# Kernel tuning notes

Measured on AMD Instinct MI355X. Metric: run time of the kernel, lower is better.

## Reference

```python
import jax, jax.numpy as jnp
import numpy as np
from jax import lax

# ---- fake-quant helpers (brevitas-style per-tensor float scaling, STE round) ----
EPS = 1e-8

def _ste_round(x):
    return x + lax.stop_gradient(jnp.round(x) - x)

def _scale(x, qmax):
    s = lax.stop_gradient(jnp.max(jnp.abs(x))) / qmax
    return jnp.maximum(s, EPS)

def fq(x, scale, qmin, qmax):
    # fake-quantize: round-to-nearest with straight-through estimator, clip, dequant
    return jnp.clip(_ste_round(x / scale), qmin, qmax) * scale

def quant_act_int8(x):
    s = _scale(x, 127.0)
    return fq(x, s, -128.0, 127.0), s

def quant_weight_int4(w):
    # 4-bit signed, narrow range [-7, 7] (brevitas weight quant default narrow_range)
    s = _scale(w, 7.0)
    return fq(w, s, -7.0, 7.0), s

def quant_relu_uint4(x):
    y = jax.nn.relu(x)
    s = _scale(y, 15.0)
    return fq(y, s, 0.0, 15.0)

def quant_bias_int32(b, scale):
    # Int32Bias: bias quantized at input_scale * weight_scale
    return _ste_round(b / scale) * scale

def conv2d_same(x, w):
    # NCHW, OIHW, padding=1, stride=1
    return lax.conv_general_dilated(x, w, window_strides=(1, 1), padding=((1, 1), (1, 1)),
                                    dimension_numbers=('NCHW', 'OIHW', 'NCHW'))

def maxpool2(x):
    return lax.reduce_window(x, -jnp.inf, lax.max, (1, 1, 2, 2), (1, 1, 2, 2), 'VALID')

def quant_conv(x, w, b):
    xq, sx = quant_act_int8(x)        # input_quant: Int8ActPerTensorFloat
    wq, sw = quant_weight_int4(w)     # weight_bit_width=4
    bq = quant_bias_int32(b, sx * sw) # bias_quant: Int32Bias
    y = conv2d_same(xq, wq) + bq[None, :, None, None]
    yq, _ = quant_act_int8(y)         # output_quant: Int8ActPerTensorFloat
    return yq

def quant_linear(x, w, b):
    xq, sx = quant_act_int8(x)
    wq, sw = quant_weight_int4(w)
    bq = quant_bias_int32(b, sx * sw)
    y = xq @ wq.T + bq
    yq, _ = quant_act_int8(y)
    return yq


def setup_inputs() -> dict:
    key = jax.random.key(0)
    ks = jax.random.split(key, 7)
    B = 8192
    x = jax.random.normal(ks[0], (B, 1, 28, 28), dtype=jnp.float32)
    w1 = jax.random.normal(ks[1], (16, 1, 3, 3), dtype=jnp.float32) * 0.3
    b1 = jax.random.normal(ks[2], (16,), dtype=jnp.float32) * 0.1
    w2 = jax.random.normal(ks[3], (32, 16, 3, 3), dtype=jnp.float32) * 0.1
    b2 = jax.random.normal(ks[4], (32,), dtype=jnp.float32) * 0.1
    wf = jax.random.normal(ks[5], (10, 32 * 7 * 7), dtype=jnp.float32) * 0.05
    bf = jax.random.normal(ks[6], (10,), dtype=jnp.float32) * 0.1
    return {'x': x, 'w1': w1, 'b1': b1, 'w2': w2, 'b2': b2, 'wf': wf, 'bf': bf}


def reference(x, w1, b1, w2, b2, wf, bf):
    h, _ = quant_act_int8(x)              # inputQuant
    h = quant_conv(h, w1, b1)             # conv1
    h = quant_relu_uint4(h)               # relu1 (4-bit)
    h = maxpool2(h)                       # pool1 -> [B,16,14,14]
    h = quant_conv(h, w2, b2)             # conv2
    h = quant_relu_uint4(h)               # relu2
    h = maxpool2(h)                       # pool2 -> [B,32,7,7]
    h = h.reshape(h.shape[0], -1)         # flatten -> [B,1568]
    return quant_linear(h, wf, bf)        # fc -> [B,10]
```

## Files before the change

kernel.cpp:

```cpp
#include <hip/hip_runtime.h>
#include <climits>

#define NB 8192
#define EPSQ 1e-8f

using i32x4  = __attribute__((ext_vector_type(4)))  int;
using i32x16 = __attribute__((ext_vector_type(16))) int;

#define WS_F(ws)     ((float*)(ws))
#define WS_I(ws)     ((int*)((char*)(ws)+128))
#define WS_B1L(ws)   ((int*)((char*)(ws)+384))
#define WS_B2L(ws)   ((int*)((char*)(ws)+448))
#define WS_BFL(ws)   ((int*)((char*)(ws)+576))
#define WS_M1F(ws)   ((float*)((char*)(ws)+640))
#define WS_B1F(ws)   ((float*)((char*)(ws)+1280))
#define WS_B2FR(ws)  ((char*)(ws)+2048)
#define WS_Q2TAB(ws) ((signed char*)((char*)(ws)+7168))
#define WS_Q3TAB(ws) ((signed char*)((char*)(ws)+7424))
#define WS_B1FR(ws)  ((char*)(ws)+7680)
#define WS_MFF(ws)   ((float*)((char*)(ws)+20480))
#define WS_WFP(ws)   ((char*)(ws)+83200)
#define WS_RA1(ws)   ((int*)((char*)(ws)+139264))
#define WS_RS1(ws)   ((int*)((char*)(ws)+164352))
#define WS_RA2(ws)   ((int*)((char*)(ws)+189440))
#define WS_RS2(ws)   ((int*)((char*)(ws)+197632))
#define WS_RA3(ws)   ((int*)((char*)(ws)+205824))
#define WS_RAX(ws)   ((float*)((char*)(ws)+206848))
#define WS_WMX(ws)   ((float*)((char*)(ws)+215040))
#define WS_Q2B(ws)   ((signed char*)((char*)(ws)+215552))
#define WS_BIG_OFF   281600

__device__ __forceinline__ float clampf(float v, float lo, float hi){ return fminf(fmaxf(v, lo), hi); }

__device__ __forceinline__ float wave_max_f(float v){
#pragma unroll
  for (int off=32; off; off>>=1) v = fmaxf(v, __shfl_down(v, off, 64));
  return v;
}
__device__ __forceinline__ int wave_max_i(int v){
#pragma unroll
  for (int off=32; off; off>>=1) v = max(v, __shfl_down(v, off, 64));
  return v;
}

__device__ __forceinline__ void reduce2_atomic(int amax, int smax, int* gA, int* gS){
  amax = wave_max_i(amax); smax = wave_max_i(smax);
  __shared__ int sA[4], sS[4];
  int w = threadIdx.x>>6, l = threadIdx.x&63;
  if (l==0){ sA[w]=amax; sS[w]=smax; }
  __syncthreads();
  if (threadIdx.x==0){
#pragma unroll
    for (int i=1;i<4;i++){ amax=max(amax,sA[i]); smax=max(smax,sS[i]); }
    atomicMax(gA, amax); atomicMax(gS, smax);
  }
}

__device__ __forceinline__ void reduce2_store(int amax, int smax, int* pA, int* pS){
  amax = wave_max_i(amax); smax = wave_max_i(smax);
  __shared__ int sA[4], sS[4];
  int w = threadIdx.x>>6, l = threadIdx.x&63;
  if (l==0){ sA[w]=amax; sS[w]=smax; }
  __syncthreads();
  if (threadIdx.x==0){
#pragma unroll
    for (int i=1;i<4;i++){ amax=max(amax,sA[i]); smax=max(smax,sS[i]); }
    *pA = amax; *pS = smax;
  }
}

__global__ void k_init(char* ws){
  int* I = WS_I(ws);
  if (threadIdx.x==0){ I[0]=0; I[1]=0; I[2]=INT_MIN; I[3]=0; I[4]=INT_MIN; I[5]=0; }
}

__global__ void k_absx(const float* __restrict__ x, char* ws){
  const float4* x4 = (const float4*)x;
  const int n4 = NB*784/4;
  float m = 0.f;
  for (int i = blockIdx.x*blockDim.x + threadIdx.x; i < n4; i += gridDim.x*blockDim.x){
    float4 v = x4[i];
    m = fmaxf(m, fmaxf(fmaxf(fabsf(v.x),fabsf(v.y)), fmaxf(fabsf(v.z),fabsf(v.w))));
  }
  m = wave_max_f(m);
  __shared__ float sm[4];
  int w = threadIdx.x>>6;
  if ((threadIdx.x&63)==0) sm[w]=m;
  __syncthreads();
  if (threadIdx.x==0){
    m = fmaxf(fmaxf(sm[0],sm[1]), fmaxf(sm[2],sm[3]));
    WS_RAX(ws)[blockIdx.x] = m;
  }
}

__global__ void k_absxw(const float* __restrict__ x,
                        const float* __restrict__ w1, const float* __restrict__ w2,
                        const float* __restrict__ wf, char* ws){
  __shared__ float red[256];
  int b = blockIdx.x, t = threadIdx.x;
  if (b < 81){
    float m = 0.f;
    if (b==0){ if (t<144) m = fabsf(w1[t]); }
    else if (b<19){ m = fabsf(w2[(b-1)*256 + t]); }
    else { int i=(b-19)*256+t; if (i<15680) m = fabsf(wf[i]); }
    red[t]=m; __syncthreads();
    for (int s=128;s;s>>=1){ if (t<s) red[t]=fmaxf(red[t],red[t+s]); __syncthreads(); }
    if (t==0) WS_WMX(ws)[b]=red[0];
    return;
  }
  const int xb = b - 81;
  const float4* x4 = (const float4*)x;
  const int n4 = NB*784/4;
  float m = 0.f;
  for (int i = xb*256 + t; i < n4; i += 2048*256){
    float4 v = x4[i];
    m = fmaxf(m, fmaxf(fmaxf(fabsf(v.x),fabsf(v.y)), fmaxf(fabsf(v.z),fabsf(v.w))));
  }
  m = wave_max_f(m);
  __shared__ float sm[4];
  int w = t>>6;
  if ((t&63)==0) sm[w]=m;
  __syncthreads();
  if (t==0){
    m = fmaxf(fmaxf(sm[0],sm[1]), fmaxf(sm[2],sm[3]));
    WS_RAX(ws)[xb] = m;
  }
}

__global__ void k_wmax(const float* __restrict__ w1, const float* __restrict__ w2,
                       const float* __restrict__ wf, char* ws){
  __shared__ float red[256];
  int b = blockIdx.x, t = threadIdx.x;
  float m = 0.f;
  if (b==0){ if (t<144) m = fabsf(w1[t]); }
  else if (b<19){ m = fabsf(w2[(b-1)*256 + t]); }
  else { int i=(b-19)*256+t; if (i<15680) m = fabsf(wf[i]); }
  red[t]=m; __syncthreads();
  for (int s=128;s;s>>=1){ if (t<s) red[t]=fmaxf(red[t],red[t+s]); __syncthreads(); }
  if (t==0) WS_WMX(ws)[b]=red[0];
}

__global__ void k_scales(const float* __restrict__ w1, const float* __restrict__ b1, char* ws){
  __shared__ float red[256];
  float* F = WS_F(ws);
  int t = threadIdx.x;
  float vw1 = WS_WMX(ws)[0];
  float m2=0.f, mf=0.f;
  if (t<18) m2 = WS_WMX(ws)[1+t];
  if (t<62) mf = WS_WMX(ws)[19+t];
  red[t]=m2; __syncthreads();
  for (int s=128;s;s>>=1){ if (t<s) red[t]=fmaxf(red[t],red[t+s]); __syncthreads(); }
  float mw2=red[0]; __syncthreads();
  red[t]=mf; __syncthreads();
  for (int s=128;s;s>>=1){ if (t<s) red[t]=fmaxf(red[t],red[t+s]); __syncthreads(); }
  float mwf=red[0]; __syncthreads();
  float mxv=0.f;
  for (int i=t;i<2048;i+=256) mxv=fmaxf(mxv,WS_RAX(ws)[i]);
  red[t]=mxv; __syncthreads();
  for (int s=128;s;s>>=1){ if (t<s) red[t]=fmaxf(red[t],red[t+s]); __syncthreads(); }
  float mx=red[0]; __syncthreads();

  float s0  = fmaxf(mx/127.f, EPSQ);
  float sx1 = fmaxf((127.f*s0)/127.f, EPSQ);
  float sw1 = fmaxf(vw1/7.f, EPSQ);
  float sw2 = fmaxf(mw2/7.f, EPSQ);
  float swf = fmaxf(mwf/7.f, EPSQ);
  float sb1 = sx1*sw1;
  if (t==0){ F[0]=s0; F[1]=sx1; F[2]=sw1; F[3]=sb1; F[7]=sw2; F[12]=swf; }
  if (t<144) WS_M1F(ws)[t] = clampf(rintf(w1[t]/sw1), -7.f, 7.f);
  if (t<16){
    int bl = (int)rintf(b1[t]/sb1);
    WS_B1L(ws)[t] = bl;
    WS_B1F(ws)[t] = (float)bl;
  }
}

__global__ void k_pack(const float* __restrict__ w1, const float* __restrict__ w2,
                       const float* __restrict__ wf, char* ws){
  const float* F = WS_F(ws);
  int id = blockIdx.x*256 + threadIdx.x;
  if (id < 5120){
    float sw2 = F[7];
    int chunk=id>>10, r=id&1023, ln=r>>4, j=r&15;
    int tap=2*chunk+(ln>>5), oc=ln&31;
    signed char v=0;
    if (tap<9) v=(signed char)clampf(rintf(w2[oc*144 + j*9 + tap]/sw2), -7.f, 7.f);
    WS_B2FR(ws)[id]=v;
  } else if (id < 6144){
    float sw1 = F[2];
    int i=id-5120;
    int ln=i>>4, j=i&15;
    int k=(ln>>5)*16+j, oc=ln&31;
    signed char v=0;
    if (k<9 && oc<16) v=(signed char)clampf(rintf(w1[oc*9+k]/sw1), -7.f, 7.f);
    WS_B1FR(ws)[i]=v;
  } else if (id < 56320){
    float swf = F[12];
    int i=id-6144;
    int chunk=i>>10, r2=i&1023, ln=r2>>4, j=r2&15;
    int oc=ln&31, k=chunk*32+(ln>>5)*16+j;
    int cell=k>>5, ch=k&31;
    signed char v=0;
    if (oc<10) v=(signed char)clampf(rintf(wf[oc*1568 + ch*49 + cell]/swf), -7.f, 7.f);
    ((signed char*)WS_WFP(ws))[i]=v;
  } else if (id < 72000){
    float swf = F[12];
    int i=id-56320;
    WS_MFF(ws)[i] = clampf(rintf(wf[i]/swf), -7.f, 7.f);
  }
}

__global__ void k_wq(const float* __restrict__ w1, const float* __restrict__ b1,
                     const float* __restrict__ w2, const float* __restrict__ wf,
                     char* ws){
  __shared__ float red[256];
  float* F = WS_F(ws);
  int t = threadIdx.x;
  auto bmaxabs = [&](const float* p, int n)->float{
    float m=0.f; for (int i=t;i<n;i+=256) m=fmaxf(m,fabsf(p[i]));
    red[t]=m; __syncthreads();
    for (int s=128;s;s>>=1){ if (t<s) red[t]=fmaxf(red[t],red[t+s]); __syncthreads(); }
    float r=red[0]; __syncthreads(); return r;
  };
  float mw1 = bmaxabs(w1,144);
  float mw2 = bmaxabs(w2,4608);
  float mwf = bmaxabs(wf,15680);
  float mxv=0.f;
  for (int i=t;i<2048;i+=256) mxv=fmaxf(mxv,WS_RAX(ws)[i]);
  red[t]=mxv; __syncthreads();
  for (int s=128;s;s>>=1){ if (t<s) red[t]=fmaxf(red[t],red[t+s]); __syncthreads(); }
  float mx=red[0]; __syncthreads();

  float s0  = fmaxf(mx/127.f, EPSQ);
  float sx1 = fmaxf((127.f*s0)/127.f, EPSQ);
  float sw1 = fmaxf(mw1/7.f, EPSQ);
  float sw2 = fmaxf(mw2/7.f, EPSQ);
  float swf = fmaxf(mwf/7.f, EPSQ);
  float sb1 = sx1*sw1;
  if (t==0){ F[0]=s0; F[1]=sx1; F[2]=sw1; F[3]=sb1; F[7]=sw2; F[12]=swf; }
  float* m1f = WS_M1F(ws);
  for (int i=t;i<144;i+=256) m1f[i] = clampf(rintf(w1[i]/sw1), -7.f, 7.f);
  if (t<16){
    int bl = (int)rintf(b1[t]/sb1);
    WS_B1L(ws)[t] = bl;
    WS_B1F(ws)[t] = (float)bl;
  }
  for (int i=t;i<5120;i+=256){
    int chunk=i>>10, r=i&1023, ln=r>>4, j=r&15;
    int tap=2*chunk+(ln>>5), oc=ln&31;
    signed char v=0;
    if (tap<9) v=(signed char)clampf(rintf(w2[oc*144 + j*9 + tap]/sw2), -7.f, 7.f);
    WS_B2FR(ws)[i]=v;
  }
  for (int i=t;i<1024;i+=256){
    int ln=i>>4, j=i&15;
    int k=(ln>>5)*16+j, oc=ln&31;
    signed char v=0;
    if (k<9 && oc<16) v=(signed char)clampf(rintf(w1[oc*9+k]/sw1), -7.f, 7.f);
    WS_B1FR(ws)[i]=v;
  }
  float* mff = WS_MFF(ws);
  for (int i=t;i<15680;i+=256) mff[i] = clampf(rintf(wf[i]/swf), -7.f, 7.f);
  for (int i=t;i<50176;i+=256){
    int chunk=i>>10, r2=i&1023, ln=r2>>4, j=r2&15;
    int oc=ln&31, k=chunk*32+(ln>>5)*16+j;
    int cell=k>>5, ch=k&31;
    signed char v=0;
    if (oc<10) v=(signed char)clampf(rintf(wf[oc*1568 + ch*49 + cell]/swf), -7.f, 7.f);
    ((signed char*)WS_WFP(ws))[i]=v;
  }
}

template<bool FULLR>
__global__ void k_s1(const float* __restrict__ b2, char* ws){
  float* F=WS_F(ws); int* I=WS_I(ws);
  __shared__ int rA[256], rS[256];
  __shared__ float sh[4];
  int t=threadIdx.x;
  int amaxI, smaxI;
  if constexpr (FULLR){
    int a=0, s=INT_MIN;
    const int* ra=WS_RA1(ws); const int* rs=WS_RS1(ws);
    for (int i=t;i<6272;i+=256){ a=max(a,ra[i]); s=max(s,rs[i]); }
    rA[t]=a; rS[t]=s; __syncthreads();
    for (int st=128;st;st>>=1){ if (t<st){ rA[t]=max(rA[t],rA[t+st]); rS[t]=max(rS[t],rS[t+st]); } __syncthreads(); }
    amaxI=rA[0]; smaxI=rS[0];
  } else { amaxI=I[1]; smaxI=I[2]; }
  if (t==0){
    float sb1=F[3];
    float sy1 = fmaxf((sb1*(float)amaxI)/127.f, EPSQ);
    float mp  = sb1*(float)smaxI;
    float P1  = clampf(rintf(mp/sy1), 0.f, 127.f);
    float sr1 = fmaxf((sy1*P1)/15.f, EPSQ);
    float N1  = clampf(rintf((sy1*P1)/sr1), 0.f, 15.f);
    float sx2 = fmaxf((N1*sr1)/127.f, EPSQ);
    float sb2 = sx2*F[7];
    F[4]=sy1; F[5]=sr1; F[6]=sx2; F[8]=sb2;
    sh[0]=sy1; sh[1]=sr1; sh[2]=sx2; sh[3]=sb2;
  }
  __syncthreads();
  float sy1=sh[0], sr1=sh[1], sx2=sh[2], sb2=sh[3];
  int k = t-128;
  float n = (k>0) ? clampf(rintf((sy1*(float)k)/sr1), 0.f, 15.f) : 0.f;
  WS_Q2TAB(ws)[t] = (signed char)clampf(rintf((n*sr1)/sx2), -128.f, 127.f);
  if (t<32) WS_B2L(ws)[t] = (int)rintf(b2[t]/sb2);
}

__global__ void k_s1q2(const float* __restrict__ b2, char* ws){
  float* F=WS_F(ws);
  __shared__ int rA[256], rS[256];
  int t=threadIdx.x;
  int a=0, s=INT_MIN;
  const int* ra=WS_RA1(ws); const int* rs=WS_RS1(ws);
  for (int i=t;i<6272;i+=256){ a=max(a,ra[i]); s=max(s,rs[i]); }
  rA[t]=a; rS[t]=s; __syncthreads();
  for (int st=128;st;st>>=1){ if (t<st){ rA[t]=max(rA[t],rA[t+st]); rS[t]=max(rS[t],rS[t+st]); } __syncthreads(); }
  int amaxI=rA[0], smaxI=rS[0];
  float sb1=F[3];
  float sy1 = fmaxf((sb1*(float)amaxI)/127.f, EPSQ);
  float P1  = clampf(rintf((sb1*(float)smaxI)/sy1), 0.f, 127.f);
  float sr1 = fmaxf((sy1*P1)/15.f, EPSQ);
  float N1  = clampf(rintf((sy1*P1)/sr1), 0.f, 15.f);
  float sx2 = fmaxf((N1*sr1)/127.f, EPSQ);
  float sb2 = sx2*F[7];
  if (blockIdx.x==0){
    if (t==0){ F[4]=sy1; F[5]=sr1; F[6]=sx2; F[8]=sb2; }
    if (t<32) WS_B2L(ws)[t] = (int)rintf(b2[t]/sb2);
  }
  int idx = blockIdx.x*256 + t;
  int m = idx - 32768;
  float k1 = clampf(rintf((sb1*(float)m)/sy1), -128.f, 127.f);
  float n  = (k1>0.f) ? clampf(rintf((sy1*k1)/sr1), 0.f, 15.f) : 0.f;
  WS_Q2B(ws)[idx] = (signed char)clampf(rintf((n*sr1)/sx2), -128.f, 127.f);
}

template<bool FULLR>
__global__ void k_s2(const float* __restrict__ bf, char* ws){
  float* F=WS_F(ws); int* I=WS_I(ws);
  __shared__ int rA[256], rS[256];
  __shared__ float sh[4];
  int t=threadIdx.x;
  int amaxI, smaxI;
  if constexpr (FULLR){
    int a=0, s=INT_MIN;
    const int* ra=WS_RA2(ws); const int* rs=WS_RS2(ws);
    for (int i=t;i<2048;i+=256){ a=max(a,ra[i]); s=max(s,rs[i]); }
    rA[t]=a; rS[t]=s; __syncthreads();
    for (int st=128;st;st>>=1){ if (t<st){ rA[t]=max(rA[t],rA[t+st]); rS[t]=max(rS[t],rS[t+st]); } __syncthreads(); }
    amaxI=rA[0]; smaxI=rS[0];
  } else { amaxI=I[3]; smaxI=I[4]; }
  if (t==0){
    float sb2=F[8];
    float sy2 = fmaxf((sb2*(float)amaxI)/127.f, EPSQ);
    float mp  = sb2*(float)smaxI;
    float P2  = clampf(rintf(mp/sy2), 0.f, 127.f);
    float sr2 = fmaxf((sy2*P2)/15.f, EPSQ);
    float N2  = clampf(rintf((sy2*P2)/sr2), 0.f, 15.f);
    float sx3 = fmaxf((N2*sr2)/127.f, EPSQ);
    float sb3 = sx3*F[12];
    F[9]=sy2; F[10]=sr2; F[11]=sx3; F[13]=sb3;
    sh[0]=sy2; sh[1]=sr2; sh[2]=sx3; sh[3]=sb3;
  }
  __syncthreads();
  float sy2=sh[0], sr2=sh[1], sx3=sh[2], sb3=sh[3];
  int k = t-128;
  float n = (k>0) ? clampf(rintf((sy2*(float)k)/sr2), 0.f, 15.f) : 0.f;
  WS_Q3TAB(ws)[t] = (signed char)clampf(rintf((n*sr2)/sx3), -128.f, 127.f);
  if (t<16) WS_BFL(ws)[t] = (t<10) ? (int)rintf(bf[t]/sb3) : 0;
}

template<bool FULLR>
__global__ void k_s3(char* ws){
  float* F=WS_F(ws); int* I=WS_I(ws);
  __shared__ int rA[256];
  int t=threadIdx.x;
  int amaxI;
  if constexpr (FULLR){
    rA[t] = WS_RA3(ws)[t];
    __syncthreads();
    for (int st=128;st;st>>=1){ if (t<st) rA[t]=max(rA[t],rA[t+st]); __syncthreads(); }
    amaxI = rA[0];
  } else { amaxI = I[5]; }
  if (t==0) F[14] = fmaxf((F[13]*(float)amaxI)/127.f, EPSQ);
}

__global__ __launch_bounds__(256) void k_conv1f(const float* __restrict__ x,
                                                char* __restrict__ ws,
                                                short* __restrict__ i1p){
  const int t = threadIdx.x;
  const int id = blockIdx.x*256 + t;
  const int img = id/196, cell = id - img*196;
  const int py = cell/14, px = cell - py*14;
  const float s0 = WS_F(ws)[0];
  const float* xi = x + img*784;
  const int r0 = 2*py-1, c0 = 2*px-1;
  float in[4][4];
#pragma unroll
  for (int rr=0; rr<4; rr++){
    int r = r0+rr;
    bool rv = (unsigned)r < 28u;
#pragma unroll
    for (int cc=0; cc<4; cc++){
      int c = c0+cc;
      float v = 0.f;
      if (rv && (unsigned)c < 28u) v = xi[r*28+c];
      in[rr][cc] = v;
    }
  }
#pragma unroll
  for (int rr=0; rr<4; rr++)
#pragma unroll
    for (int cc=0; cc<4; cc++)
      in[rr][cc] = clampf(rintf(in[rr][cc]/s0), -128.f, 127.f);

  const float* __restrict__ m1f = WS_M1F(ws);
  const float* __restrict__ b1f = WS_B1F(ws);
  int amax=0, smax=INT_MIN;
  short outv[16];
#pragma unroll
  for (int oc=0; oc<16; oc++){
    float b = b1f[oc];
    float a00=b, a01=b, a10=b, a11=b;
#pragma unroll
    for (int dy=0; dy<3; dy++){
#pragma unroll
      for (int dx=0; dx<3; dx++){
        float wt = m1f[oc*9+dy*3+dx];
        a00 = fmaf(in[dy  ][dx  ], wt, a00);
        a01 = fmaf(in[dy  ][dx+1], wt, a01);
        a10 = fmaf(in[dy+1][dx  ], wt, a10);
        a11 = fmaf(in[dy+1][dx+1], wt, a11);
      }
    }
    int v00=(int)a00, v01=(int)a01, v10=(int)a10, v11=(int)a11;
    int mx = max(max(v00,v01), max(v10,v11));
    int ax = max(max(v00<0?-v00:v00, v01<0?-v01:v01), max(v10<0?-v10:v10, v11<0?-v11:v11));
    amax = max(amax, ax);
    smax = max(smax, mx);
    outv[oc] = (short)mx;
  }
  int4* dst = (int4*)(i1p + (size_t)id*16);
  dst[0] = *(const int4*)&outv[0];
  dst[1] = *(const int4*)&outv[8];
  reduce2_store(amax, smax, &WS_RA1(ws)[blockIdx.x], &WS_RS1(ws)[blockIdx.x]);
}

__global__ __launch_bounds__(256) void k_conv2r(char* __restrict__ ws,
                                                short* __restrict__ i1p,
                                                int* __restrict__ p2g){
  __shared__ __align__(16) signed char q2p4[4][4096];
  const int t=threadIdx.x, lane=t&63, wid=t>>6;
  const int img = blockIdx.x*4 + wid;
  signed char* q2p = q2p4[wid];
  const signed char* __restrict__ q2b = WS_Q2B(ws);

#pragma unroll
  for (int k=0;k<8;k++) ((unsigned long long*)q2p)[lane + 64*k] = 0ULL;

  const unsigned* src = (const unsigned*)(i1p + (size_t)img*3136);
#pragma unroll
  for (int k=0;k<24;k++){
    int idx = lane + 64*k;
    unsigned wv = src[idx];
    int e0 = idx*2;
    int cellc = e0 >> 4, ch = e0 & 15;
    int pyc = cellc/14, pxc = cellc - pyc*14;
    int m0 = (int)(short)(wv & 0xFFFFu);
    int m1 = (int)(short)(wv >> 16);
    int b0 = (int)(unsigned char)q2b[m0+32768];
    int b1 = (int)(unsigned char)q2b[m1+32768];
    *(unsigned short*)(q2p + ((pyc+1)*16 + (pxc+1))*16 + ch) = (unsigned short)(b0 | (b1<<8));
  }
  if (lane < 32){
    int idx = 1536 + lane;
    unsigned wv = src[idx];
    int e0 = idx*2;
    int cellc = e0 >> 4, ch = e0 & 15;
    int pyc = cellc/14, pxc = cellc - pyc*14;
    int m0 = (int)(short)(wv & 0xFFFFu);
    int m1 = (int)(short)(wv >> 16);
    int b0 = (int)(unsigned char)q2b[m0+32768];
    int b1 = (int)(unsigned char)q2b[m1+32768];
    *(unsigned short*)(q2p + ((pyc+1)*16 + (pxc+1))*16 + ch) = (unsigned short)(b0 | (b1<<8));
  }

  i32x4 bfr[5];
  const i32x4* bg = (const i32x4*)WS_B2FR(ws);
#pragma unroll
  for (int c=0;c<5;c++) bfr[c] = bg[c*64+lane];
  const int col = lane&31, h = lane>>5;
  const int bias = WS_B2L(ws)[col];
  int amax2=0, smax2=INT_MIN;
  const int TOFF[9] = {0,1,2,16,17,18,32,33,34};
  int* dstb = p2g + (size_t)img*1568;

#pragma unroll
  for (int mt=0; mt<7; mt++){
    int m = mt*32 + col;
    int g = m>>2, sub = m&3;
    bool gv = g < 49;
    int py = (g*37)>>8;
    int px = g - py*7;
    int oy = 2*py + (sub>>1), ox = 2*px + (sub&1);
    int E0 = oy*16 + ox;
    i32x16 acc;
#pragma unroll
    for (int r=0;r<16;r++) acc[r] = bias;
#pragma unroll
    for (int c=0;c<5;c++){
      const int t0 = TOFF[2*c];
      const int t1 = (2*c+1<9) ? TOFF[2*c+1] : -1;
      int toff = h ? t1 : t0;
      int entry = (gv && toff>=0) ? (E0 + toff) : 0;
      i32x4 a = *(const i32x4*)(q2p + entry*16);
      acc = __builtin_amdgcn_mfma_i32_32x32x32_i8(a, bfr[c], acc, 0,0,0);
    }
#pragma unroll
    for (int i=0;i<4;i++){
      int gg = mt*8 + 2*i + h;
      if (gg < 49){
        int v0=acc[4*i], v1=acc[4*i+1], v2=acc[4*i+2], v3=acc[4*i+3];
        int a0=v0<0?-v0:v0, a1=v1<0?-v1:v1, a2=v2<0?-v2:v2, a3=v3<0?-v3:v3;
        amax2 = max(amax2, max(max(a0,a1),max(a2,a3)));
        int mx = max(max(v0,v1),max(v2,v3));
        smax2 = max(smax2, mx);
        dstb[gg*32 + col] = mx;
      }
    }
  }
  reduce2_store(amax2, smax2, &WS_RA2(ws)[blockIdx.x], &WS_RS2(ws)[blockIdx.x]);
}

__global__ void k_rq2(const char* __restrict__ ws, const int* __restrict__ p2g,
                      signed char* __restrict__ q3g){
  const float* F = (const float*)ws;
  const float sb2 = F[8], sy2 = F[9];
  const signed char* q3t = WS_Q3TAB(ws);
  int id = blockIdx.x*256 + threadIdx.x;
  i32x4 m4 = ((const i32x4*)p2g)[id];
  unsigned out=0;
#pragma unroll
  for (int j=0;j<4;j++){
    float k2 = clampf(rintf((sb2*(float)m4[j])/sy2), -128.f, 127.f);
    out |= ((unsigned)(unsigned char)q3t[(int)k2+128]) << (8*j);
  }
  ((unsigned*)q3g)[id] = out;
}

__global__ __launch_bounds__(256) void k_fc(char* __restrict__ ws,
                                            const signed char* __restrict__ q3g,
                                            int* __restrict__ i3out){
  __shared__ int part[3][16][64];
  int t=threadIdx.x, lane=t&63, wid=t>>6;
  int mt = blockIdx.x;
  const int col=lane&31, h=lane>>5;
  const signed char* A0 = q3g + (size_t)(mt*32 + col)*1568 + 16*h;
  const i32x4* wfp = (const i32x4*)WS_WFP(ws);
  i32x16 acc;
#pragma unroll
  for (int r=0;r<16;r++) acc[r]=0;
#pragma unroll
  for (int cc=0; cc<13; cc++){
    int c = wid + cc*4;
    if (c < 49){
      i32x4 a = *(const i32x4*)(A0 + c*32);
      i32x4 b = wfp[c*64 + lane];
      acc = __builtin_amdgcn_mfma_i32_32x32x32_i8(a, b, acc, 0,0,0);
    }
  }
  if (wid>0){
#pragma unroll
    for (int r=0;r<16;r++) part[wid-1][r][lane] = acc[r];
  }
  __syncthreads();
  if (wid==0){
    int bias = (col<10) ? WS_BFL(ws)[col] : 0;
    int am=0;
#pragma unroll
    for (int r=0;r<16;r++){
      int v = acc[r] + part[0][r][lane] + part[1][r][lane] + part[2][r][lane] + bias;
      int row=(r&3)+8*(r>>2)+4*h;
      int img = mt*32+row;
      if (col<10){
        i3out[img*10+col] = v;
        am = max(am, v<0?-v:v);
      }
    }
    am = wave_max_i(am);
    if (lane==0) WS_RA3(ws)[blockIdx.x] = am;
  }
}

__global__ void k_out2(char* __restrict__ ws, float* __restrict__ out){
  __shared__ int rA[256];
  int t=threadIdx.x;
  rA[t] = WS_RA3(ws)[t];
  __syncthreads();
  for (int st=128;st;st>>=1){ if (t<st) rA[t]=max(rA[t],rA[t+st]); __syncthreads(); }
  float sb3 = WS_F(ws)[13];
  float sy3 = fmaxf((sb3*(float)rA[0])/127.f, EPSQ);
  int i = blockIdx.x*256 + t;
  if (i < NB*10){
    int iv = ((const int*)out)[i];
    float y = sb3*(float)iv;
    float q = clampf(rintf(y/sy3), -128.f, 127.f);
    out[i] = q*sy3;
  }
}

__global__ __launch_bounds__(256) void k_c1(const float* __restrict__ x, char* __restrict__ ws,
                                            short* __restrict__ i1p){
  constexpr int OFF_K0=0, OFF_A=960, OFF_I1=13760, OFF_B1=38848;
  __shared__ __align__(16) char arena[38912];
  signed char* k0b = (signed char*)(arena+OFF_K0);
  signed char* Abuf= (signed char*)(arena+OFF_A);
  short*       I1s = (short*)(arena+OFF_I1);
  int*         b1i = (int*)(arena+OFF_B1);

  const int tid=threadIdx.x, img=blockIdx.x;
  const int lane=tid&63, wid=tid>>6;
  const float s0 = WS_F(ws)[0];

  if (tid<16) b1i[tid]=WS_B1L(ws)[tid];
  for (int i=tid;i<240;i+=256) ((int*)k0b)[i]=0;
  for (int i=tid;i<3200;i+=256) ((int*)Abuf)[i]=0;
  __syncthreads();
  const float* xi = x + img*784;
  for (int i=tid;i<784;i+=256){
    int r=i/28, c=i-r*28;
    float v = clampf(rintf(xi[i]/s0), -128.f, 127.f);
    k0b[(r+1)*32 + (c+1)] = (signed char)v;
  }
  __syncthreads();
  for (int p=tid;p<784;p+=256){
    int oy=p/28, ox=p-oy*28;
    int base = oy*32+ox;
    int al = base & ~3, sh = (base&3)*8;
    unsigned l0a=*(const unsigned*)(k0b+al),    l1a=*(const unsigned*)(k0b+al+4);
    unsigned l0b=*(const unsigned*)(k0b+al+32), l1b=*(const unsigned*)(k0b+al+36);
    unsigned l0c=*(const unsigned*)(k0b+al+64), l1c=*(const unsigned*)(k0b+al+68);
    unsigned u0=(unsigned)(((((unsigned long long)l1a)<<32)|l0a)>>sh);
    unsigned u1=(unsigned)(((((unsigned long long)l1b)<<32)|l0b)>>sh);
    unsigned u2=(unsigned)(((((unsigned long long)l1c)<<32)|l0c)>>sh);
    i32x4 row;
    row[0]=(int)((u0&0xFFFFFFu)|(u1<<24));
    row[1]=(int)(((u1>>8)&0xFFFFu)|((u2&0xFFFFu)<<16));
    row[2]=(int)((u2>>16)&0xFFu);
    row[3]=0;
    *(i32x4*)(Abuf + p*16) = row;
  }
  __syncthreads();
  const i32x4 bfr = ((const i32x4*)WS_B1FR(ws))[lane];
  const int col=lane&31, h=lane>>5;
  const int bias=(col<16)? b1i[col] : 0;
  int amax=0, smax=INT_MIN;
  for (int mt=wid; mt<25; mt+=4){
    i32x4 a={0,0,0,0};
    if (h==0) a = *(const i32x4*)(Abuf + (mt*32+col)*16);
    i32x16 acc;
#pragma unroll
    for (int r=0;r<16;r++) acc[r]=bias;
    acc=__builtin_amdgcn_mfma_i32_32x32x32_i8(a,bfr,acc,0,0,0);
#pragma unroll
    for (int r=0;r<16;r++){
      int row=(r&3)+8*(r>>2)+4*h;
      int p=mt*32+row;
      if (p<784 && col<16){
        int v=acc[r];
        amax=max(amax,v<0?-v:v); smax=max(smax,v);
        I1s[p*16+col]=(short)v;
      }
    }
  }
  __syncthreads();
  for (int i=tid;i<3136;i+=256){
    int pp=i>>4, c=i&15, py=pp/14, px=pp-py*14;
    int p0=py*56+px*2;
    int m=max(max((int)I1s[p0*16+c],(int)I1s[(p0+1)*16+c]),
              max((int)I1s[(p0+28)*16+c],(int)I1s[(p0+29)*16+c]));
    i1p[(size_t)img*3136 + i]=(short)m;
  }
  reduce2_atomic(amax,smax,&WS_I(ws)[1],&WS_I(ws)[2]);
}

template<bool FIN>
__global__ __launch_bounds__(256) void k_c2(char* __restrict__ ws, const short* __restrict__ i1p,
                                            int* __restrict__ i3out){
  constexpr int OFF_Q2L=0, OFF_B2I=3136, OFF_Q2T=3264, OFF_N2=3520,
                OFF_Q3T=9792, OFF_BFS=10048, OFF_Q3F=10112, OFF_RED=16384;
  constexpr int ARENA = FIN ? 16544 : 3520;
  __shared__ __align__(16) char arena[ARENA];
  signed char* q2l=(signed char*)(arena+OFF_Q2L);
  int* b2li=(int*)(arena+OFF_B2I);
  signed char* q2t=(signed char*)(arena+OFF_Q2T);

  const int tid=threadIdx.x, img=blockIdx.x;
  const int lane=tid&63, wid=tid>>6;
  const float* F=WS_F(ws);
  const float sb1=F[3], sy1=F[4];

  q2t[tid]=WS_Q2TAB(ws)[tid];
  if (tid<32) b2li[tid]=WS_B2L(ws)[tid];
  if constexpr (FIN){
    ((signed char*)(arena+OFF_Q3T))[tid]=WS_Q3TAB(ws)[tid];
    if (tid<16) ((int*)(arena+OFF_BFS))[tid]=WS_BFL(ws)[tid];
  }
  __syncthreads();
  for (int i=tid;i<3136;i+=256){
    int m=(int)i1p[(size_t)img*3136+i];
    float k1=clampf(rintf((sb1*(float)m)/sy1),-128.f,127.f);
    q2l[i]=q2t[(int)k1+128];
  }
  __syncthreads();

  i32x4 bfr[5];
  {
    const i32x4* bg=(const i32x4*)WS_B2FR(ws);
#pragma unroll
    for (int c=0;c<5;c++) bfr[c]=bg[c*64+lane];
  }
  const int col=lane&31, h=lane>>5;
  const int bias=b2li[col];
  int amax2=0, smax2=INT_MIN;
  float sb2=0.f, sy2=0.f;
  signed char* n2buf=nullptr;
  if constexpr (FIN){ sb2=F[8]; sy2=F[9]; n2buf=(signed char*)(arena+OFF_N2); }

  for (int mt=wid; mt<7; mt+=4){
    const int p=mt*32+col;
    const bool pv=p<196;
    const int oy=p/14, ox=p-oy*14;
    i32x16 acc;
#pragma unroll
    for (int r=0;r<16;r++) acc[r]=bias;
#pragma unroll
    for (int c=0;c<5;c++){
      const int tap=2*c+h;
      i32x4 a={0,0,0,0};
      if (pv && tap<9){
        const int iy=oy+tap/3-1, ix=ox+tap-(tap/3)*3-1;
        if ((unsigned)iy<14u && (unsigned)ix<14u) a=*(const i32x4*)(q2l+(iy*14+ix)*16);
      }
      acc=__builtin_amdgcn_mfma_i32_32x32x32_i8(a,bfr[c],acc,0,0,0);
    }
#pragma unroll
    for (int r=0;r<16;r++){
      const int row=(r&3)+8*(r>>2)+4*h;
      const int pp=mt*32+row;
      if (pp<196){
        const int v=acc[r];
        if constexpr (!FIN){ amax2=max(amax2,v<0?-v:v); smax2=max(smax2,v); }
        else {
          n2buf[col*196+pp]=(signed char)clampf(rintf((sb2*(float)v)/sy2),-128.f,127.f);
        }
      }
    }
  }
  if constexpr (!FIN){
    reduce2_atomic(amax2,smax2,&WS_I(ws)[3],&WS_I(ws)[4]);
    return;
  } else {
    __syncthreads();
    signed char* q3t_s=(signed char*)(arena+OFF_Q3T);
    float* q3f=(float*)(arena+OFF_Q3F);
    for (int i=tid;i<1568;i+=256){
      int cch=i/49, s=i-cch*49, qy=s/7, qx=s-qy*7;
      int b=cch*196+qy*28+qx*2;
      int m=max(max((int)n2buf[b],(int)n2buf[b+1]),max((int)n2buf[b+14],(int)n2buf[b+15]));
      q3f[i]=(float)q3t_s[m+128];
    }
    __syncthreads();
    const float* mff=WS_MFF(ws);
    float a10[10];
#pragma unroll
    for (int o=0;o<10;o++) a10[o]=0.f;
    for (int k=tid;k<1568;k+=256){
      float qa=q3f[k];
#pragma unroll
      for (int o=0;o<10;o++) a10[o]=fmaf(qa,mff[o*1568+k],a10[o]);
    }
#pragma unroll
    for (int o=0;o<10;o++){
#pragma unroll
      for (int off=32;off;off>>=1) a10[o]+=__shfl_down(a10[o],off,64);
    }
    float* redf=(float*)(arena+OFF_RED);
    int* bfs=(int*)(arena+OFF_BFS);
    if (lane==0){
#pragma unroll
      for (int o=0;o<10;o++) redf[wid*10+o]=a10[o];
    }
    __syncthreads();
    if (tid<10){
      float s=redf[tid]+redf[10+tid]+redf[20+tid]+redf[30+tid];
      int I3v=(int)s+bfs[tid];
      i3out[img*10+tid]=I3v;
      redf[tid]=(float)(I3v<0?-I3v:I3v);
    }
    __syncthreads();
    if (tid==0){
      int m=0;
#pragma unroll
      for (int o=0;o<10;o++) m=max(m,(int)redf[o]);
      atomicMax(&WS_I(ws)[5],m);
    }
  }
}

__global__ void k_out(char* ws, float* __restrict__ out){
  float* F=WS_F(ws);
  float sb3=F[13], sy3=F[14];
  int i = blockIdx.x*blockDim.x + threadIdx.x;
  if (i < NB*10){
    int iv = ((const int*)out)[i];
    float y = sb3*(float)iv;
    float q = clampf(rintf(y/sy3), -128.f, 127.f);
    out[i] = q*sy3;
  }
}

extern "C" void kernel_launch(void* const* d_in, const int* in_sizes, int n_in,
                              void* d_out, int out_size, void* d_ws, size_t ws_size,
                              hipStream_t stream){
  const float* x  = (const float*)d_in[0];
  const float* w1 = (const float*)d_in[1];
  const float* b1 = (const float*)d_in[2];
  const float* w2 = (const float*)d_in[3];
  const float* b2 = (const float*)d_in[4];
  const float* wf = (const float*)d_in[5];
  const float* bf = (const float*)d_in[6];
  char* ws = (char*)d_ws;
  float* out = (float*)d_out;
  int* i3 = (int*)d_out;

  const size_t QX_SZ  = (size_t)NB*960;
  const size_t I1_SZ  = (size_t)NB*6272;
  const size_t Q3_SZ  = (size_t)NB*1568;
  const size_t needFull = (size_t)WS_BIG_OFF + QX_SZ + I1_SZ + Q3_SZ;

  if (ws_size >= needFull){
    short*       i1p = (short*)(ws + WS_BIG_OFF + QX_SZ);
    int*         p2g = (int*)i1p;
    signed char* q3g = (signed char*)(ws + WS_BIG_OFF + QX_SZ + I1_SZ);
    k_absxw <<<dim3(2129), dim3(256), 0, stream>>>(x, w1, w2, wf, ws);
    k_scales<<<dim3(1), dim3(256), 0, stream>>>(w1, b1, ws);
    k_pack  <<<dim3(282), dim3(256), 0, stream>>>(w1, w2, wf, ws);
    k_conv1f<<<dim3(NB*196/256), dim3(256), 0, stream>>>(x, ws, i1p);
    k_s1q2  <<<dim3(256), dim3(256), 0, stream>>>(b2, ws);
    k_conv2r<<<dim3(NB/4), dim3(256), 0, stream>>>(ws, i1p, p2g);
    k_s2<true><<<dim3(1), dim3(256), 0, stream>>>(bf, ws);
    k_rq2   <<<dim3(NB*1568/1024), dim3(256), 0, stream>>>(ws, p2g, q3g);
    k_fc    <<<dim3(256), dim3(256), 0, stream>>>(ws, q3g, i3);
    k_out2  <<<dim3((NB*10+255)/256), dim3(256), 0, stream>>>(ws, out);
  } else {
    short* i1p = (short*)(ws + WS_BIG_OFF);
    k_init<<<dim3(1), dim3(64), 0, stream>>>(ws);
    k_absx<<<dim3(2048), dim3(256), 0, stream>>>(x, ws);
    k_wq  <<<dim3(1), dim3(256), 0, stream>>>(w1, b1, w2, wf, ws);
    k_c1<<<dim3(NB), dim3(256), 0, stream>>>(x, ws, i1p);
    k_s1<false><<<dim3(1), dim3(256), 0, stream>>>(b2, ws);
    k_c2<false><<<dim3(NB), dim3(256), 0, stream>>>(ws, i1p, i3);
    k_s2<false><<<dim3(1), dim3(256), 0, stream>>>(bf, ws);
    k_c2<true ><<<dim3(NB), dim3(256), 0, stream>>>(ws, i1p, i3);
    k_s3<false><<<dim3(1), dim3(256), 0, stream>>>(ws);
    k_out<<<dim3((NB*10+255)/256), dim3(256), 0, stream>>>(ws, out);
  }
}
```

Measured before the change: 123.3 us.

## Pre-quantize input to padded int8 buffer and compute conv1 with sdot4

Adds a kernel that quantizes the input once into a zero-padded int8 image buffer (30x32 per image), then rewrites conv1 to read packed bytes and compute 3-tap rows with the integer sdot4 builtin against int8-packed weights prepared in k_scales. This replaces per-thread float division, rounding and 36 FMAs per channel, done redundantly on overlapping input windows, with a few dot4 instructions on shared data. It adds an extra kernel launch and a write and read of the int8 buffer. It also deletes the unused k_wmax kernel.

```diff
diff --git a/kernel.cpp b/kernel.cpp
--- a/kernel.cpp
+++ b/kernel.cpp
@@ -14,6 +14,7 @@
 #define WS_BFL(ws)   ((int*)((char*)(ws)+576))
 #define WS_M1F(ws)   ((float*)((char*)(ws)+640))
 #define WS_B1F(ws)   ((float*)((char*)(ws)+1280))
+#define WS_W1P(ws)   ((unsigned*)((char*)(ws)+1408))
 #define WS_B2FR(ws)  ((char*)(ws)+2048)
 #define WS_Q2TAB(ws) ((signed char*)((char*)(ws)+7168))
 #define WS_Q3TAB(ws) ((signed char*)((char*)(ws)+7424))
@@ -32,6 +33,10 @@
 
 __device__ __forceinline__ float clampf(float v, float lo, float hi){ return fminf(fmaxf(v, lo), hi); }
 
+__device__ __forceinline__ int dot4(unsigned a, unsigned b, int c){
+  return __builtin_amdgcn_sdot4((int)a, (int)b, c, false);
+}
+
 __device__ __forceinline__ float wave_max_f(float v){
 #pragma unroll
   for (int off=32; off; off>>=1) v = fmaxf(v, __shfl_down(v, off, 64));
@@ -125,19 +130,6 @@
     m = fmaxf(fmaxf(sm[0],sm[1]), fmaxf(sm[2],sm[3]));
     WS_RAX(ws)[xb] = m;
   }
-}
-
-__global__ void k_wmax(const float* __restrict__ w1, const float* __restrict__ w2,
-                       const float* __restrict__ wf, char* ws){
-  __shared__ float red[256];
-  int b = blockIdx.x, t = threadIdx.x;
-  float m = 0.f;
-  if (b==0){ if (t<144) m = fabsf(w1[t]); }
-  else if (b<19){ m = fabsf(w2[(b-1)*256 + t]); }
-  else { int i=(b-19)*256+t; if (i<15680) m = fabsf(wf[i]); }
-  red[t]=m; __syncthreads();
-  for (int s=128;s;s>>=1){ if (t<s) red[t]=fmaxf(red[t],red[t+s]); __syncthreads(); }
-  if (t==0) WS_WMX(ws)[b]=red[0];
 }
 
 __global__ void k_scales(const float* __restrict__ w1, const float* __restrict__ b1, char* ws){
@@ -172,6 +164,15 @@
     int bl = (int)rintf(b1[t]/sb1);
     WS_B1L(ws)[t] = bl;
     WS_B1F(ws)[t] = (float)bl;
+  }
+  __syncthreads();
+  if (t<48){
+    int oc = t/3, row = t - oc*3;
+    const float* m = WS_M1F(ws) + oc*9 + row*3;
+    unsigned b0 = (unsigned)(unsigned char)(signed char)(int)m[0];
+    unsigned bb1 = (unsigned)(unsigned char)(signed char)(int)m[1];
+    unsigned b2c = (unsigned)(unsigned char)(signed char)(int)m[2];
+    WS_W1P(ws)[t] = b0 | (bb1<<8) | (b2c<<16);
   }
 }
 
@@ -384,57 +385,60 @@
   if (t==0) F[14] = fmaxf((F[13]*(float)amaxI)/127.f, EPSQ);
 }
 
-__global__ __launch_bounds__(256) void k_conv1f(const float* __restrict__ x,
+__global__ void k_qx(const float* __restrict__ x, const char* __restrict__ ws,
+                     signed char* __restrict__ qx){
+  const float s0 = ((const float*)ws)[0];
+  int id = blockIdx.x*256 + threadIdx.x;
+  int img = id/240, w = id - img*240;
+  int r = w>>3, c4 = (w&7)<<2;
+  const float* xi = x + img*784;
+  unsigned out = 0;
+#pragma unroll
+  for (int j=0;j<4;j++){
+    int c = c4+j;
+    bool valid = (r>=1) && (r<=28) && (c>=1) && (c<=28);
+    int q = 0;
+    if (valid){
+      float xv = xi[(r-1)*28 + (c-1)];
+      q = (int)clampf(rintf(xv/s0), -128.f, 127.f);
+    }
+    out |= ((unsigned)(unsigned char)(signed char)q) << (8*j);
+  }
+  ((unsigned*)qx)[id] = out;
+}
+
+__global__ __launch_bounds__(256) void k_conv1d(const signed char* __restrict__ qx,
                                                 char* __restrict__ ws,
                                                 short* __restrict__ i1p){
   const int t = threadIdx.x;
   const int id = blockIdx.x*256 + t;
   const int img = id/196, cell = id - img*196;
   const int py = cell/14, px = cell - py*14;
-  const float s0 = WS_F(ws)[0];
-  const float* xi = x + img*784;
-  const int r0 = 2*py-1, c0 = 2*px-1;
-  float in[4][4];
+  const signed char* qb = qx + img*960 + (2*py)*32;
+  const int pc0 = 2*px;
+  const int al = pc0 & ~3, sh = (pc0&3)*8;
+  unsigned wrd[4], whi[4];
 #pragma unroll
   for (int rr=0; rr<4; rr++){
-    int r = r0+rr;
-    bool rv = (unsigned)r < 28u;
-#pragma unroll
-    for (int cc=0; cc<4; cc++){
-      int c = c0+cc;
-      float v = 0.f;
-      if (rv && (unsigned)c < 28u) v = xi[r*28+c];
-      in[rr][cc] = v;
-    }
-  }
-#pragma unroll
-  for (int rr=0; rr<4; rr++)
-#pragma unroll
-    for (int cc=0; cc<4; cc++)
-      in[rr][cc] = clampf(rintf(in[rr][cc]/s0), -128.f, 127.f);
-
-  const float* __restrict__ m1f = WS_M1F(ws);
-  const float* __restrict__ b1f = WS_B1F(ws);
+    unsigned lo = *(const unsigned*)(qb + rr*32 + al);
+    unsigned hi = *(const unsigned*)(qb + rr*32 + al + 4);
+    wrd[rr] = (unsigned)(((((unsigned long long)hi)<<32)|lo) >> sh);
+    whi[rr] = wrd[rr] >> 8;
+  }
+  const unsigned* __restrict__ w1p = WS_W1P(ws);
+  const int* __restrict__ b1l = WS_B1L(ws);
   int amax=0, smax=INT_MIN;
   short outv[16];
 #pragma unroll
   for (int oc=0; oc<16; oc++){
-    float b = b1f[oc];
-    float a00=b, a01=b, a10=b, a11=b;
-#pragma unroll
-    for (int dy=0; dy<3; dy++){
-#pragma unroll
-      for (int dx=0; dx<3; dx++){
-        float wt = m1f[oc*9+dy*3+dx];
-        a00 = fmaf(in[dy  ][dx  ], wt, a00);
-        a01 = fmaf(in[dy  ][dx+1], wt, a01);
-        a10 = fmaf(in[dy+1][dx  ], wt, a10);
-        a11 = fmaf(in[dy+1][dx+1], wt, a11);
-      }
-    }
-    int v00=(int)a00, v01=(int)a01, v10=(int)a10, v11=(int)a11;
-    int mx = max(max(v00,v01), max(v10,v11));
-    int ax = max(max(v00<0?-v00:v00, v01<0?-v01:v01), max(v10<0?-v10:v10, v11<0?-v11:v11));
+    unsigned w0 = w1p[oc*3], w1 = w1p[oc*3+1], w2 = w1p[oc*3+2];
+    int bl = b1l[oc];
+    int a00 = dot4(wrd[2], w2, dot4(wrd[1], w1, dot4(wrd[0], w0, bl)));
+    int a01 = dot4(whi[2], w2, dot4(whi[1], w1, dot4(whi[0], w0, bl)));
+    int a10 = dot4(wrd[3], w2, dot4(wrd[2], w1, dot4(wrd[1], w0, bl)));
+    int a11 = dot4(whi[3], w2, dot4(whi[2], w1, dot4(whi[1], w0, bl)));
+    int mx = max(max(a00,a01), max(a10,a11));
+    int ax = max(max(a00<0?-a00:a00, a01<0?-a01:a01), max(a10<0?-a10:a10, a11<0?-a11:a11));
     amax = max(amax, ax);
     smax = max(smax, mx);
     outv[oc] = (short)mx;
@@ -839,13 +843,15 @@
   const size_t needFull = (size_t)WS_BIG_OFF + QX_SZ + I1_SZ + Q3_SZ;
 
   if (ws_size >= needFull){
+    signed char* qx  = (signed char*)(ws + WS_BIG_OFF);
     short*       i1p = (short*)(ws + WS_BIG_OFF + QX_SZ);
     int*         p2g = (int*)i1p;
     signed char* q3g = (signed char*)(ws + WS_BIG_OFF + QX_SZ + I1_SZ);
     k_absxw <<<dim3(2129), dim3(256), 0, stream>>>(x, w1, w2, wf, ws);
     k_scales<<<dim3(1), dim3(256), 0, stream>>>(w1, b1, ws);
+    k_qx    <<<dim3(NB*240/256), dim3(256), 0, stream>>>(x, ws, qx);
     k_pack  <<<dim3(282), dim3(256), 0, stream>>>(w1, w2, wf, ws);
-    k_conv1f<<<dim3(NB*196/256), dim3(256), 0, stream>>>(x, ws, i1p);
+    k_conv1d<<<dim3(NB*196/256), dim3(256), 0, stream>>>(qx, ws, i1p);
     k_s1q2  <<<dim3(256), dim3(256), 0, stream>>>(b2, ws);
     k_conv2r<<<dim3(NB/4), dim3(256), 0, stream>>>(ws, i1p, p2g);
     k_s2<true><<<dim3(1), dim3(256), 0, stream>>>(bf, ws);
```

Result: faster. 118.8 us (-3.7%).
